# Performance work log

Measured on AMD Instinct MI355X. Metric: run time of the kernel, lower is better.

## Reference

```python
import jax, jax.numpy as jnp
import numpy as np

D_MODEL = 768
NHEAD = 12
D_K = D_MODEL // NHEAD


def setup_inputs() -> dict:
    key = jax.random.key(0)
    ks = jax.random.split(key, 9)
    s = 1.0 / np.sqrt(D_MODEL)
    x = jax.random.normal(ks[0], (2, 4096, D_MODEL), dtype=jnp.float32)
    Wq = jax.random.uniform(ks[1], (D_MODEL, D_MODEL), jnp.float32, -s, s)
    bq = jax.random.uniform(ks[2], (D_MODEL,), jnp.float32, -s, s)
    Wk = jax.random.uniform(ks[3], (D_MODEL, D_MODEL), jnp.float32, -s, s)
    bk = jax.random.uniform(ks[4], (D_MODEL,), jnp.float32, -s, s)
    Wv = jax.random.uniform(ks[5], (D_MODEL, D_MODEL), jnp.float32, -s, s)
    bv = jax.random.uniform(ks[6], (D_MODEL,), jnp.float32, -s, s)
    Wo = jax.random.uniform(ks[7], (D_MODEL, D_MODEL), jnp.float32, -s, s)
    bo = jax.random.uniform(ks[8], (D_MODEL,), jnp.float32, -s, s)
    return {"x": x, "Wq": Wq, "bq": bq, "Wk": Wk, "bk": bk,
            "Wv": Wv, "bv": bv, "Wo": Wo, "bo": bo}


def reference(x, Wq, bq, Wk, bk, Wv, bv, Wo, bo):
    B, S, _ = x.shape
    # Linear layers: torch nn.Linear(y) = y @ W.T + b; weights stored [out,in]
    def split_heads(y):  # [B,S,D] -> [B,H,S,dk]
        return y.reshape(B, S, NHEAD, D_K).transpose(0, 2, 1, 3)
    Q = split_heads(x @ Wq.T + bq)
    K = split_heads(x @ Wk.T + bk)
    V = split_heads(x @ Wv.T + bv)
    scores = jnp.einsum('bhqd,bhkd->bhqk', Q, K) / jnp.sqrt(jnp.float32(D_K))
    attn = jax.nn.softmax(scores, axis=-1)
    context = jnp.einsum('bhqk,bhkd->bhqd', attn, V)
    context = context.transpose(0, 2, 1, 3).reshape(B, S, D_MODEL)
    return context @ Wo.T + bo
```

## Files before the change

### kernel.cpp

```cpp
#include <hip/hip_runtime.h>
#include <hip/hip_bf16.h>
#include <cstdint>

typedef __bf16 bf16;
typedef bf16 bf16x8 __attribute__((ext_vector_type(8)));
typedef float f32x4 __attribute__((ext_vector_type(4)));

#define MFMA16(a, b, c) __builtin_amdgcn_mfma_f32_16x16x32_bf16((a), (b), (c), 0, 0, 0)

constexpr int D_MODEL = 768;
constexpr int NHEAD = 12;
constexpr int DK = 64;
constexpr int SEQ = 4096;
constexpr int BATCH = 2;
constexpr int MROWS = BATCH * SEQ;
constexpr float QSCALE = 0.125f * 1.44269504089f;

__global__ __launch_bounds__(256, 2) void gemm_qkv(const float* __restrict__ X,
                                                   const float* __restrict__ Wq,
                                                   const float* __restrict__ Wk,
                                                   const float* __restrict__ Wv,
                                                   const float* __restrict__ bq,
                                                   const float* __restrict__ bk,
                                                   const float* __restrict__ bv,
                                                   bf16* __restrict__ Qb,
                                                   bf16* __restrict__ Kb,
                                                   bf16* __restrict__ Vtb) {
    constexpr int LDP = 88;
    __shared__ bf16 Asm[128][LDP];
    __shared__ bf16 Bsm[128][LDP];
    const int tid = threadIdx.x, lane = tid & 63, wid = tid >> 6;
    const int wm = wid >> 1, wn = wid & 1;
    const int m0 = blockIdx.x * 128;
    const int sel = blockIdx.y / 6;
    const int n0 = (blockIdx.y % 6) * 128;
    const float* Bw = sel == 0 ? Wq : (sel == 1 ? Wk : Wv);
    const float* bias = sel == 0 ? bq : (sel == 1 ? bk : bv);

    f32x4 acc[4][4];
#pragma unroll
    for (int i = 0; i < 4; i++)
#pragma unroll
        for (int j = 0; j < 4; j++) acc[i][j] = f32x4{0.f, 0.f, 0.f, 0.f};

    const int rr = tid >> 3, cc = (tid & 7) * 8;
    for (int k0 = 0; k0 < 768; k0 += 64) {
#pragma unroll
        for (int p = 0; p < 4; p++) {
            const float* src = X + (size_t)(m0 + p * 32 + rr) * 768 + k0 + cc;
            const float4 f0 = *reinterpret_cast<const float4*>(src);
            const float4 f1 = *reinterpret_cast<const float4*>(src + 4);
            bf16x8 a8;
            a8[0] = (bf16)f0.x; a8[1] = (bf16)f0.y; a8[2] = (bf16)f0.z; a8[3] = (bf16)f0.w;
            a8[4] = (bf16)f1.x; a8[5] = (bf16)f1.y; a8[6] = (bf16)f1.z; a8[7] = (bf16)f1.w;
            *reinterpret_cast<bf16x8*>(&Asm[p * 32 + rr][cc]) = a8;
        }
#pragma unroll
        for (int p = 0; p < 4; p++) {
            const float* src = Bw + (size_t)(n0 + p * 32 + rr) * 768 + k0 + cc;
            const float4 f0 = *reinterpret_cast<const float4*>(src);
            const float4 f1 = *reinterpret_cast<const float4*>(src + 4);
            bf16x8 b8;
            b8[0] = (bf16)f0.x; b8[1] = (bf16)f0.y; b8[2] = (bf16)f0.z; b8[3] = (bf16)f0.w;
            b8[4] = (bf16)f1.x; b8[5] = (bf16)f1.y; b8[6] = (bf16)f1.z; b8[7] = (bf16)f1.w;
            *reinterpret_cast<bf16x8*>(&Bsm[p * 32 + rr][cc]) = b8;
        }
        __syncthreads();
#pragma unroll
        for (int kk = 0; kk < 64; kk += 32) {
            const int krd = kk + ((lane >> 4) << 3);
            bf16x8 af[4], bfr[4];
#pragma unroll
            for (int i = 0; i < 4; i++)
                af[i] = *reinterpret_cast<const bf16x8*>(&Asm[wm * 64 + i * 16 + (lane & 15)][krd]);
#pragma unroll
            for (int j = 0; j < 4; j++)
                bfr[j] = *reinterpret_cast<const bf16x8*>(&Bsm[wn * 64 + j * 16 + (lane & 15)][krd]);
#pragma unroll
            for (int i = 0; i < 4; i++)
#pragma unroll
                for (int j = 0; j < 4; j++) acc[i][j] = MFMA16(af[i], bfr[j], acc[i][j]);
        }
        __syncthreads();
    }

    const float scale = (sel == 0) ? QSCALE : 1.0f;
    const int rbase = m0 + wm * 64 + ((lane >> 4) << 2);
    const int cbase = n0 + wn * 64 + (lane & 15);
    bf16* obf = sel == 0 ? Qb : (sel == 1 ? Kb : Vtb);
#pragma unroll
    for (int i = 0; i < 4; i++) {
#pragma unroll
        for (int j = 0; j < 4; j++) {
            const int ncol = cbase + j * 16;
            const float bv = bias[ncol];
            const int h = ncol >> 6, d = ncol & 63;
#pragma unroll
            for (int r = 0; r < 4; r++) {
                const int mrow = rbase + i * 16 + r;
                const float v = (acc[i][j][r] + bv) * scale;
                const int b = mrow >> 12, s = mrow & 4095;
                if (sel < 2) {
                    obf[(((size_t)(b * NHEAD + h)) * SEQ + s) * DK + d] = (bf16)v;
                } else {
                    const int sp = (s & ~63) | (((s & 15) << 2) | ((s >> 4) & 3));
                    obf[(((size_t)(b * NHEAD + h)) * DK + d) * SEQ + sp] = (bf16)v;
                }
            }
        }
    }
}

__global__ __launch_bounds__(256, 2) void gemm_out(const bf16* __restrict__ A,
                                                   const float* __restrict__ Bw,
                                                   const float* __restrict__ bias,
                                                   float* __restrict__ ofl) {
    constexpr int LDP = 88;
    __shared__ bf16 Asm[128][LDP];
    __shared__ bf16 Bsm[128][LDP];
    const int tid = threadIdx.x, lane = tid & 63, wid = tid >> 6;
    const int wm = wid >> 1, wn = wid & 1;
    const int m0 = blockIdx.x * 128, n0 = blockIdx.y * 128;

    f32x4 acc[4][4];
#pragma unroll
    for (int i = 0; i < 4; i++)
#pragma unroll
        for (int j = 0; j < 4; j++) acc[i][j] = f32x4{0.f, 0.f, 0.f, 0.f};

    const int rr = tid >> 3, cc = (tid & 7) * 8;
    for (int k0 = 0; k0 < 768; k0 += 64) {
#pragma unroll
        for (int p = 0; p < 4; p++)
            *reinterpret_cast<bf16x8*>(&Asm[p * 32 + rr][cc]) =
                *reinterpret_cast<const bf16x8*>(A + (size_t)(m0 + p * 32 + rr) * 768 + k0 + cc);
#pragma unroll
        for (int p = 0; p < 4; p++) {
            const float* src = Bw + (size_t)(n0 + p * 32 + rr) * 768 + k0 + cc;
            const float4 f0 = *reinterpret_cast<const float4*>(src);
            const float4 f1 = *reinterpret_cast<const float4*>(src + 4);
            bf16x8 b8;
            b8[0] = (bf16)f0.x; b8[1] = (bf16)f0.y; b8[2] = (bf16)f0.z; b8[3] = (bf16)f0.w;
            b8[4] = (bf16)f1.x; b8[5] = (bf16)f1.y; b8[6] = (bf16)f1.z; b8[7] = (bf16)f1.w;
            *reinterpret_cast<bf16x8*>(&Bsm[p * 32 + rr][cc]) = b8;
        }
        __syncthreads();
#pragma unroll
        for (int kk = 0; kk < 64; kk += 32) {
            const int krd = kk + ((lane >> 4) << 3);
            bf16x8 af[4], bfr[4];
#pragma unroll
            for (int i = 0; i < 4; i++)
                af[i] = *reinterpret_cast<const bf16x8*>(&Asm[wm * 64 + i * 16 + (lane & 15)][krd]);
#pragma unroll
            for (int j = 0; j < 4; j++)
                bfr[j] = *reinterpret_cast<const bf16x8*>(&Bsm[wn * 64 + j * 16 + (lane & 15)][krd]);
#pragma unroll
            for (int i = 0; i < 4; i++)
#pragma unroll
                for (int j = 0; j < 4; j++) acc[i][j] = MFMA16(af[i], bfr[j], acc[i][j]);
        }
        __syncthreads();
    }

    const int rbase = m0 + wm * 64 + ((lane >> 4) << 2);
    const int cbase = n0 + wn * 64 + (lane & 15);
#pragma unroll
    for (int i = 0; i < 4; i++) {
#pragma unroll
        for (int j = 0; j < 4; j++) {
            const int ncol = cbase + j * 16;
            const float bv = bias[ncol];
#pragma unroll
            for (int r = 0; r < 4; r++) {
                const int mrow = rbase + i * 16 + r;
                ofl[(size_t)mrow * 768 + ncol] = acc[i][j][r] + bv;
            }
        }
    }
}

__global__ __launch_bounds__(256, 3) void attn_kernel(const bf16* __restrict__ Qb,
                                                      const bf16* __restrict__ Kb,
                                                      const bf16* __restrict__ Vtb,
                                                      bf16* __restrict__ ctx) {
    __shared__ bf16 Ksm[64][72];
    __shared__ bf16 Vts[64][72];
    __shared__ bf16 Psm[4][32][72];
    const int tid = threadIdx.x, l = tid & 63, w = tid >> 6;
    const int bh = blockIdx.y;
    const int q0 = blockIdx.x * 128;
    const bf16* Qh = Qb + (size_t)bh * SEQ * DK;
    const bf16* Kh = Kb + (size_t)bh * SEQ * DK;
    const bf16* Vth = Vtb + (size_t)bh * DK * SEQ;

    const int rsel = l & 15, csel = l >> 4;

    bf16x8 qf[2][2];
#pragma unroll
    for (int qi = 0; qi < 2; qi++) {
        const int qr = q0 + w * 32 + qi * 16 + rsel;
#pragma unroll
        for (int kk = 0; kk < 2; kk++)
            qf[qi][kk] = *reinterpret_cast<const bf16x8*>(Qh + (size_t)qr * DK + kk * 32 + csel * 8);
    }

    bf16x8 vones;
    {
        const bf16 ov = (rsel == 0) ? (bf16)1.0f : (bf16)0.0f;
#pragma unroll
        for (int j = 0; j < 8; j++) vones[j] = ov;
    }

    float m = -1e30f;
    f32x4 aco[2][4], aco_x[2];
#pragma unroll
    for (int qi = 0; qi < 2; qi++) {
#pragma unroll
        for (int f = 0; f < 4; f++) aco[qi][f] = f32x4{0.f, 0.f, 0.f, 0.f};
        aco_x[qi] = f32x4{0.f, 0.f, 0.f, 0.f};
    }

    const int srow = tid >> 2, sc4 = (tid & 3) * 16;

    bf16x8 pk0 = *reinterpret_cast<const bf16x8*>(Kh + (size_t)srow * DK + sc4);
    bf16x8 pk1 = *reinterpret_cast<const bf16x8*>(Kh + (size_t)srow * DK + sc4 + 8);
    bf16x8 pv0 = *reinterpret_cast<const bf16x8*>(Vth + (size_t)srow * SEQ + sc4);
    bf16x8 pv1 = *reinterpret_cast<const bf16x8*>(Vth + (size_t)srow * SEQ + sc4 + 8);

    constexpr int NT = SEQ / 64;
    for (int t = 0; t < NT; ++t) {
        __syncthreads();
        *reinterpret_cast<bf16x8*>(&Ksm[srow][sc4]) = pk0;
        *reinterpret_cast<bf16x8*>(&Ksm[srow][sc4 + 8]) = pk1;
        *reinterpret_cast<bf16x8*>(&Vts[srow][sc4]) = pv0;
        *reinterpret_cast<bf16x8*>(&Vts[srow][sc4 + 8]) = pv1;
        __syncthreads();

        if (t + 1 < NT) {
            const int kn = (t + 1) * 64;
            pk0 = *reinterpret_cast<const bf16x8*>(Kh + (size_t)(kn + srow) * DK + sc4);
            pk1 = *reinterpret_cast<const bf16x8*>(Kh + (size_t)(kn + srow) * DK + sc4 + 8);
            pv0 = *reinterpret_cast<const bf16x8*>(Vth + (size_t)srow * SEQ + kn + sc4);
            pv1 = *reinterpret_cast<const bf16x8*>(Vth + (size_t)srow * SEQ + kn + sc4 + 8);
        }

        f32x4 s4[2][4];
#pragma unroll
        for (int qi = 0; qi < 2; qi++)
#pragma unroll
            for (int f = 0; f < 4; f++) s4[qi][f] = f32x4{0.f, 0.f, 0.f, 0.f};
#pragma unroll
        for (int kk = 0; kk < 2; kk++) {
            const int krd = kk * 32 + csel * 8;
#pragma unroll
            for (int f = 0; f < 4; f++) {
                const bf16x8 kf = *reinterpret_cast<const bf16x8*>(&Ksm[f * 16 + rsel][krd]);
                s4[0][f] = MFMA16(qf[0][kk], kf, s4[0][f]);
                s4[1][f] = MFMA16(qf[1][kk], kf, s4[1][f]);
            }
        }

        float tm = s4[0][0][0];
#pragma unroll
        for (int qi = 0; qi < 2; qi++)
#pragma unroll
            for (int f = 0; f < 4; f++)
#pragma unroll
                for (int r = 0; r < 4; r++) tm = fmaxf(tm, s4[qi][f][r]);
        if (__any(tm - m > 8.f)) {
            tm = fmaxf(tm, __shfl_xor(tm, 1));
            tm = fmaxf(tm, __shfl_xor(tm, 2));
            tm = fmaxf(tm, __shfl_xor(tm, 4));
            tm = fmaxf(tm, __shfl_xor(tm, 8));
            tm = fmaxf(tm, __shfl_xor(tm, 16));
            tm = fmaxf(tm, __shfl_xor(tm, 32));
            const float scl = __builtin_amdgcn_exp2f(m - tm);
            m = tm;
#pragma unroll
            for (int qi = 0; qi < 2; qi++) {
#pragma unroll
                for (int f = 0; f < 4; f++)
#pragma unroll
                    for (int r = 0; r < 4; r++) aco[qi][f][r] *= scl;
#pragma unroll
                for (int r = 0; r < 4; r++) aco_x[qi][r] *= scl;
            }
        }

#pragma unroll
        for (int qi = 0; qi < 2; qi++)
#pragma unroll
            for (int r = 0; r < 4; r++) {
                union { bf16 h[4]; uint64_t u; } pk4;
#pragma unroll
                for (int f = 0; f < 4; f++)
                    pk4.h[f] = (bf16)__builtin_amdgcn_exp2f(s4[qi][f][r] - m);
                *reinterpret_cast<uint64_t*>(&Psm[w][qi * 16 + csel * 4 + r][rsel * 4]) = pk4.u;
            }

#pragma unroll
        for (int ph = 0; ph < 2; ph++) {
            const int kc = ph * 32 + csel * 8;
            const bf16x8 pf0 = *reinterpret_cast<const bf16x8*>(&Psm[w][rsel][kc]);
            const bf16x8 pf1 = *reinterpret_cast<const bf16x8*>(&Psm[w][16 + rsel][kc]);
#pragma unroll
            for (int f2 = 0; f2 < 4; f2++) {
                const bf16x8 vf = *reinterpret_cast<const bf16x8*>(&Vts[f2 * 16 + rsel][kc]);
                aco[0][f2] = MFMA16(pf0, vf, aco[0][f2]);
                aco[1][f2] = MFMA16(pf1, vf, aco[1][f2]);
            }
            aco_x[0] = MFMA16(pf0, vones, aco_x[0]);
            aco_x[1] = MFMA16(pf1, vones, aco_x[1]);
        }
    }

    const int b = bh / NHEAD, h = bh % NHEAD;
#pragma unroll
    for (int qi = 0; qi < 2; qi++) {
        float inv[4];
#pragma unroll
        for (int r = 0; r < 4; r++) inv[r] = 1.0f / __shfl(aco_x[qi][r], l & 48);
#pragma unroll
        for (int f = 0; f < 4; f++)
#pragma unroll
            for (int r = 0; r < 4; r++) {
                const int q = q0 + w * 32 + qi * 16 + csel * 4 + r;
                const int d = f * 16 + rsel;
                ctx[((size_t)b * SEQ + q) * D_MODEL + h * DK + d] = (bf16)(aco[qi][f][r] * inv[r]);
            }
    }
}

extern "C" void kernel_launch(void* const* d_in, const int* in_sizes, int n_in,
                              void* d_out, int out_size, void* d_ws, size_t ws_size,
                              hipStream_t stream) {
    const float* x  = (const float*)d_in[0];
    const float* Wq = (const float*)d_in[1];
    const float* bq = (const float*)d_in[2];
    const float* Wk = (const float*)d_in[3];
    const float* bk = (const float*)d_in[4];
    const float* Wv = (const float*)d_in[5];
    const float* bv = (const float*)d_in[6];
    const float* Wo = (const float*)d_in[7];
    const float* bo = (const float*)d_in[8];
    float* out = (float*)d_out;

    char* ws = (char*)d_ws;
    size_t off = 0;
    auto alloc = [&](size_t bytes) { void* p = ws + off; off += (bytes + 255) & ~(size_t)255; return p; };
    bf16* Qb   = (bf16*)alloc((size_t)BATCH * NHEAD * SEQ * DK * 2);
    bf16* Kb   = (bf16*)alloc((size_t)BATCH * NHEAD * SEQ * DK * 2);
    bf16* Vtb  = (bf16*)alloc((size_t)BATCH * NHEAD * SEQ * DK * 2);
    bf16* ctxb = (bf16*)alloc((size_t)MROWS * 768 * 2);

    gemm_qkv<<<dim3(MROWS / 128, 18), 256, 0, stream>>>(x, Wq, Wk, Wv, bq, bk, bv, Qb, Kb, Vtb);

    attn_kernel<<<dim3(SEQ / 128, BATCH * NHEAD), 256, 0, stream>>>(Qb, Kb, Vtb, ctxb);

    gemm_out<<<dim3(MROWS / 128, 768 / 128), 256, 0, stream>>>(ctxb, Wo, bo, out);
}
```

Measured before the change: 216.0 us.

## Load K/V fragments directly from global memory, removing LDS staging and barriers

```diff
diff --git a/kernel.cpp b/kernel.cpp
--- a/kernel.cpp
+++ b/kernel.cpp
@@ -184,8 +184,6 @@
                                                       const bf16* __restrict__ Kb,
                                                       const bf16* __restrict__ Vtb,
                                                       bf16* __restrict__ ctx) {
-    __shared__ bf16 Ksm[64][72];
-    __shared__ bf16 Vts[64][72];
     __shared__ bf16 Psm[4][32][72];
     const int tid = threadIdx.x, l = tid & 63, w = tid >> 6;
     const int bh = blockIdx.y;
@@ -221,29 +219,27 @@
         aco_x[qi] = f32x4{0.f, 0.f, 0.f, 0.f};
     }
 
-    const int srow = tid >> 2, sc4 = (tid & 3) * 16;
-
-    bf16x8 pk0 = *reinterpret_cast<const bf16x8*>(Kh + (size_t)srow * DK + sc4);
-    bf16x8 pk1 = *reinterpret_cast<const bf16x8*>(Kh + (size_t)srow * DK + sc4 + 8);
-    bf16x8 pv0 = *reinterpret_cast<const bf16x8*>(Vth + (size_t)srow * SEQ + sc4);
-    bf16x8 pv1 = *reinterpret_cast<const bf16x8*>(Vth + (size_t)srow * SEQ + sc4 + 8);
+    const bf16* kbase = Kh + (size_t)rsel * DK + csel * 8;
+    const bf16* vbase = Vth + (size_t)rsel * SEQ + csel * 8;
 
     constexpr int NT = SEQ / 64;
     for (int t = 0; t < NT; ++t) {
-        __syncthreads();
-        *reinterpret_cast<bf16x8*>(&Ksm[srow][sc4]) = pk0;
-        *reinterpret_cast<bf16x8*>(&Ksm[srow][sc4 + 8]) = pk1;
-        *reinterpret_cast<bf16x8*>(&Vts[srow][sc4]) = pv0;
-        *reinterpret_cast<bf16x8*>(&Vts[srow][sc4 + 8]) = pv1;
-        __syncthreads();
-
-        if (t + 1 < NT) {
-            const int kn = (t + 1) * 64;
-            pk0 = *reinterpret_cast<const bf16x8*>(Kh + (size_t)(kn + srow) * DK + sc4);
-            pk1 = *reinterpret_cast<const bf16x8*>(Kh + (size_t)(kn + srow) * DK + sc4 + 8);
-            pv0 = *reinterpret_cast<const bf16x8*>(Vth + (size_t)srow * SEQ + kn + sc4);
-            pv1 = *reinterpret_cast<const bf16x8*>(Vth + (size_t)srow * SEQ + kn + sc4 + 8);
-        }
+        const size_t koff = (size_t)t * 64 * DK;
+        const int voff = t * 64;
+
+        bf16x8 kf[2][4];
+#pragma unroll
+        for (int f = 0; f < 4; f++)
+#pragma unroll
+            for (int kk = 0; kk < 2; kk++)
+                kf[kk][f] = *reinterpret_cast<const bf16x8*>(kbase + koff + (size_t)f * 16 * DK + kk * 32);
+
+        bf16x8 vf[2][4];
+#pragma unroll
+        for (int ph = 0; ph < 2; ph++)
+#pragma unroll
+            for (int f2 = 0; f2 < 4; f2++)
+                vf[ph][f2] = *reinterpret_cast<const bf16x8*>(vbase + (size_t)f2 * 16 * SEQ + voff + ph * 32);
 
         f32x4 s4[2][4];
 #pragma unroll
@@ -252,12 +248,10 @@
             for (int f = 0; f < 4; f++) s4[qi][f] = f32x4{0.f, 0.f, 0.f, 0.f};
 #pragma unroll
         for (int kk = 0; kk < 2; kk++) {
-            const int krd = kk * 32 + csel * 8;
 #pragma unroll
             for (int f = 0; f < 4; f++) {
-                const bf16x8 kf = *reinterpret_cast<const bf16x8*>(&Ksm[f * 16 + rsel][krd]);
-                s4[0][f] = MFMA16(qf[0][kk], kf, s4[0][f]);
-                s4[1][f] = MFMA16(qf[1][kk], kf, s4[1][f]);
+                s4[0][f] = MFMA16(qf[0][kk], kf[kk][f], s4[0][f]);
+                s4[1][f] = MFMA16(qf[1][kk], kf[kk][f], s4[1][f]);
             }
         }
 
@@ -306,9 +300,8 @@
             const bf16x8 pf1 = *reinterpret_cast<const bf16x8*>(&Psm[w][16 + rsel][kc]);
 #pragma unroll
             for (int f2 = 0; f2 < 4; f2++) {
-                const bf16x8 vf = *reinterpret_cast<const bf16x8*>(&Vts[f2 * 16 + rsel][kc]);
-                aco[0][f2] = MFMA16(pf0, vf, aco[0][f2]);
-                aco[1][f2] = MFMA16(pf1, vf, aco[1][f2]);
+                aco[0][f2] = MFMA16(pf0, vf[ph][f2], aco[0][f2]);
+                aco[1][f2] = MFMA16(pf1, vf[ph][f2], aco[1][f2]);
             }
             aco_x[0] = MFMA16(pf0, vones, aco_x[0]);
             aco_x[1] = MFMA16(pf1, vones, aco_x[1]);
```

After: 428.8 us. +98.5%, slower.
